# Kernel tuning notes

Measured on AMD Instinct MI355X. Metric: run time of the kernel, lower is better.

Reference implementation:

```python
import jax, jax.numpy as jnp
import numpy as np

N, E, D_IN, D, D_OUT, L = 50000, 800000, 128, 256, 64, 3
TAU0 = 0.5
LN_EPS = 1e-5


def setup_inputs() -> dict:
    key = jax.random.key(0)
    ks = jax.random.split(key, 16)
    u01 = jax.random.uniform(ks[2], (L, 2, N, 2), minval=1e-6, maxval=1.0 - 1e-6)
    gumbel = -jnp.log(-jnp.log(u01))  # standard Gumbel(0,1) noise, one draw per layer per action net
    s = lambda k, shape, fan: jax.random.normal(k, shape) * np.float32(1.0 / np.sqrt(fan))
    return {
        'x': jax.random.normal(ks[0], (N, D_IN), dtype=jnp.float32),
        'edge_index': jax.random.randint(ks[1], (2, E), 0, N),
        'gumbel_noise': gumbel,
        'W_enc': s(ks[3], (D_IN, D), D_IN), 'b_enc': jnp.zeros((D,), jnp.float32),
        'W_root': s(ks[4], (L, D, D), D), 'W_agg': s(ks[5], (L, D, D), D), 'b_env': jnp.zeros((L, D), jnp.float32),
        'Wa_in_r': s(ks[6], (D, 2), D), 'Wa_in_a': s(ks[7], (D, 2), D), 'b_in': jnp.zeros((2,), jnp.float32),
        'Wa_out_r': s(ks[8], (D, 2), D), 'Wa_out_a': s(ks[9], (D, 2), D), 'b_out': jnp.zeros((2,), jnp.float32),
        'Wt_r': s(ks[10], (D, 1), D), 'Wt_a': s(ks[11], (D, 1), D), 'b_t': jnp.zeros((1,), jnp.float32),
        'ln_g': jnp.ones((D,), jnp.float32), 'ln_b': jnp.zeros((D,), jnp.float32),
        'W_dec': s(ks[12], (D, D_OUT), D), 'b_dec': jnp.zeros((D_OUT,), jnp.float32),
    }


def reference(x, edge_index, gumbel_noise, W_enc, b_enc, W_root, W_agg, b_env,
              Wa_in_r, Wa_in_a, b_in, Wa_out_r, Wa_out_a, b_out,
              Wt_r, Wt_a, b_t, ln_g, ln_b, W_dec, b_dec):
    n = x.shape[0]
    u, v = edge_index[0], edge_index[1]  # message flows v -> u (aggregate at u)

    def conv(h, Wr, Wa, b, ew=None):
        # GraphConv-style: root transform + sum-aggregated (optionally edge-weighted) neighbor transform
        msg = h[v] if ew is None else ew[:, None] * h[v]  # [E, D]
        agg = jax.ops.segment_sum(msg, u, num_segments=n)  # [N, D]
        return h @ Wr + agg @ Wa + b

    def layernorm(h):
        m = jnp.mean(h, axis=-1, keepdims=True)
        var = jnp.mean((h - m) ** 2, axis=-1, keepdims=True)
        return (h - m) * jax.lax.rsqrt(var + LN_EPS) * ln_g + ln_b

    def gumbel_hard(logits, g, temp):
        # hard gumbel-softmax with straight-through estimator, per-node temperature
        y = jax.nn.softmax((logits + g) / temp, axis=-1)
        hard = jax.nn.one_hot(jnp.argmax(y, axis=-1), 2, dtype=y.dtype)
        return hard + y - jax.lax.stop_gradient(y)

    # env encoder + (dropout=identity) + relu
    h = jax.nn.relu(x @ W_enc + b_enc)

    for l in range(W_root.shape[0]):
        h = layernorm(h)
        in_logits = conv(h, Wa_in_r, Wa_in_a, b_in)    # [N, 2]
        out_logits = conv(h, Wa_out_r, Wa_out_a, b_out)  # [N, 2]
        t = conv(h, Wt_r, Wt_a, b_t)                   # [N, 1]
        temp = 1.0 / (jax.nn.softplus(t) + TAU0)       # TempSoftPlus: per-node inverse temperature
        in_prob = gumbel_hard(in_logits, gumbel_noise[l, 0], temp)
        out_prob = gumbel_hard(out_logits, gumbel_noise[l, 1], temp)
        ew = in_prob[:, 0][u] * out_prob[:, 0][v]      # [E] gated edge weights
        h = jax.nn.relu(conv(h, W_root[l], W_agg[l], b_env[l], ew))

    h = layernorm(h)
    return h @ W_dec + b_dec
```

## Files before the change

### kernel.cpp

```cpp
#include <hip/hip_runtime.h>
#include <cstdint>

#define NN 50000
#define EE 800000
#define DIN 128
#define DD 256
#define DOUT 64
#define NLAYERS 3
#define LN_EPS 1e-5f
#define NB_SCAN ((NN + 255) / 256)

typedef __attribute__((ext_vector_type(8))) _Float16 h8;
typedef __attribute__((ext_vector_type(4))) _Float16 h4;
typedef __attribute__((ext_vector_type(4))) float f4;

__device__ __forceinline__ float red16(float v) {
  v += __shfl_xor(v, 1, 64);
  v += __shfl_xor(v, 2, 64);
  v += __shfl_xor(v, 4, 64);
  v += __shfl_xor(v, 8, 64);
  return v;
}

__device__ __forceinline__ void splith(const float4& a, const float4& b, h8& p1, h8& p2) {
  float t[8] = {a.x, a.y, a.z, a.w, b.x, b.y, b.z, b.w};
#pragma unroll
  for (int i = 0; i < 8; ++i) {
    _Float16 x = (_Float16)t[i];
    p1[i] = x;
    p2[i] = (_Float16)(t[i] - (float)x);
  }
}

__global__ void k_zero_deg(int* __restrict__ deg) {
  int i = blockIdx.x * 256 + threadIdx.x;
  if (i < NN) deg[i] = 0;
}

__global__ void k_deg(const int* __restrict__ ei, int* __restrict__ deg) {
  int e = blockIdx.x * 256 + threadIdx.x;
  if (e < EE) atomicAdd(&deg[ei[e]], 1);
}

__global__ __launch_bounds__(256) void k_scan1(const int* __restrict__ deg,
                                               int* __restrict__ bsum) {
  __shared__ int sm[256];
  const int t = threadIdx.x;
  int i = blockIdx.x * 256 + t;
  sm[t] = (i < NN) ? deg[i] : 0;
  __syncthreads();
  for (int off = 128; off > 0; off >>= 1) {
    if (t < off) sm[t] += sm[t + off];
    __syncthreads();
  }
  if (t == 0) bsum[blockIdx.x] = sm[0];
}

__global__ __launch_bounds__(256) void k_scan2(const int* __restrict__ bsum,
                                               int* __restrict__ boff,
                                               int* __restrict__ rowptr) {
  __shared__ int sm[256];
  const int t = threadIdx.x;
  int v = (t < NB_SCAN) ? bsum[t] : 0;
  sm[t] = v;
  __syncthreads();
  for (int off = 1; off < 256; off <<= 1) {
    int x = (t >= off) ? sm[t - off] : 0;
    __syncthreads();
    sm[t] += x;
    __syncthreads();
  }
  if (t < NB_SCAN) boff[t] = sm[t] - v;
  if (t == 0) rowptr[NN] = sm[255];
}

__global__ __launch_bounds__(256) void k_scan3(const int* __restrict__ deg,
                                               const int* __restrict__ boff,
                                               int* __restrict__ rowptr,
                                               int* __restrict__ cursor) {
  __shared__ int sm[256];
  const int t = threadIdx.x;
  int i = blockIdx.x * 256 + t;
  int v = (i < NN) ? deg[i] : 0;
  sm[t] = v;
  __syncthreads();
  for (int off = 1; off < 256; off <<= 1) {
    int x = (t >= off) ? sm[t - off] : 0;
    __syncthreads();
    sm[t] += x;
    __syncthreads();
  }
  if (i < NN) {
    int r = boff[blockIdx.x] + sm[t] - v;
    rowptr[i] = r;
    cursor[i] = r;
  }
}

__global__ void k_fill(const int* __restrict__ ei, int* __restrict__ cursor,
                       int* __restrict__ csr_v) {
  int e = blockIdx.x * 256 + threadIdx.x;
  if (e >= EE) return;
  int u = ei[e], v = ei[EE + e];
  int slot = atomicAdd(&cursor[u], 1);
  csr_v[slot] = v;
}

__global__ void k_prep_conv(const float* __restrict__ Wr, const float* __restrict__ Wa,
                            _Float16* __restrict__ W1, _Float16* __restrict__ W2) {
  int idx = blockIdx.x * 256 + threadIdx.x;
  if (idx >= NLAYERS * DD * 2 * DD) return;
  int l = idx >> 17;
  int rem = idx & 131071;
  int n = rem >> 9, k = rem & 511;
  float w = (k < DD) ? Wr[((size_t)l * DD + k) * DD + n]
                     : Wa[((size_t)l * DD + (k - DD)) * DD + n];
  _Float16 x = (_Float16)w;
  W1[idx] = x;
  W2[idx] = (_Float16)(w - (float)x);
}

__global__ void k_prep_ed(const float* __restrict__ We, const float* __restrict__ Wd,
                          _Float16* __restrict__ E1, _Float16* __restrict__ E2,
                          _Float16* __restrict__ D1, _Float16* __restrict__ D2) {
  int idx = blockIdx.x * 256 + threadIdx.x;
  if (idx < DIN * DD) {
    int n = idx / DIN, k = idx - n * DIN;
    float w = We[(size_t)k * DD + n];
    _Float16 x = (_Float16)w;
    E1[idx] = x;
    E2[idx] = (_Float16)(w - (float)x);
  } else if (idx < DIN * DD + DD * DOUT) {
    int j = idx - DIN * DD;
    int n = j / DD, k = j - n * DD;
    float w = Wd[(size_t)k * DOUT + n];
    _Float16 x = (_Float16)w;
    D1[j] = x;
    D2[j] = (_Float16)(w - (float)x);
  }
}

__global__ __launch_bounds__(256) void k_gates_csr(
    const int* __restrict__ rowptr, const int* __restrict__ csr_v,
    const float* __restrict__ SR, const float* __restrict__ SA,
    const float* __restrict__ gn, const float* __restrict__ b_in,
    const float* __restrict__ b_out, unsigned char* __restrict__ gin,
    unsigned char* __restrict__ gout, int l) {
  int u = blockIdx.x * 256 + threadIdx.x;
  if (u >= NN) return;
  int beg = rowptr[u], end = rowptr[u + 1];
  float4 a = make_float4(0.f, 0.f, 0.f, 0.f);
  for (int j = beg; j < end; ++j) {
    int v = csr_v[j];
    float4 s = *(const float4*)(SA + (size_t)v * 4);
    a.x += s.x; a.y += s.y; a.z += s.z; a.w += s.w;
  }
  float4 r = *(const float4*)(SR + (size_t)u * 4);
  const float* gi = gn + ((size_t)(l * 2 + 0) * NN + u) * 2;
  const float* go = gn + ((size_t)(l * 2 + 1) * NN + u) * 2;
  float li0 = r.x + a.x + b_in[0] + gi[0];
  float li1 = r.y + a.y + b_in[1] + gi[1];
  gin[u] = (li0 >= li1) ? 1 : 0;
  float lo0 = r.z + a.z + b_out[0] + go[0];
  float lo1 = r.w + a.w + b_out[1] + go[1];
  gout[u] = (lo0 >= lo1) ? 1 : 0;
}

__global__ __launch_bounds__(256) void k_wagg_csr(
    const int* __restrict__ rowptr, const int* __restrict__ csr_v,
    const unsigned char* __restrict__ gin, const unsigned char* __restrict__ gout,
    const _Float16* __restrict__ hn1, const _Float16* __restrict__ hn2,
    _Float16* __restrict__ agg1, _Float16* __restrict__ agg2) {
  const int lane = threadIdx.x & 63;
  const int u = blockIdx.x * 4 + (threadIdx.x >> 6);
  if (u >= NN) return;
  float4 acc = make_float4(0.f, 0.f, 0.f, 0.f);
  float4 acc2 = make_float4(0.f, 0.f, 0.f, 0.f);
  if (gin[u]) {
    int beg = rowptr[u], end = rowptr[u + 1];
    for (int j0 = beg; j0 < end; j0 += 64) {
      int rem = end - j0;
      int v = -1;
      if (lane < rem) v = csr_v[j0 + lane];
      int ok = (v >= 0) ? (int)gout[v] : 0;
      unsigned long long mask = __ballot(ok);
      while (mask) {
        int l0 = __builtin_ctzll(mask);
        mask &= mask - 1;
        int vv0 = __shfl(v, l0);
        const h4* p0a = (const h4*)(hn1 + (size_t)vv0 * DD + lane * 4);
        const h4* p0b = (const h4*)(hn2 + (size_t)vv0 * DD + lane * 4);
        if (mask) {
          int l1 = __builtin_ctzll(mask);
          mask &= mask - 1;
          int vv1 = __shfl(v, l1);
          const h4* p1a = (const h4*)(hn1 + (size_t)vv1 * DD + lane * 4);
          const h4* p1b = (const h4*)(hn2 + (size_t)vv1 * DD + lane * 4);
          h4 a0 = *p0a, b0 = *p0b, a1 = *p1a, b1 = *p1b;
          acc.x += (float)a0[0] + (float)b0[0]; acc.y += (float)a0[1] + (float)b0[1];
          acc.z += (float)a0[2] + (float)b0[2]; acc.w += (float)a0[3] + (float)b0[3];
          acc2.x += (float)a1[0] + (float)b1[0]; acc2.y += (float)a1[1] + (float)b1[1];
          acc2.z += (float)a1[2] + (float)b1[2]; acc2.w += (float)a1[3] + (float)b1[3];
        } else {
          h4 a0 = *p0a, b0 = *p0b;
          acc.x += (float)a0[0] + (float)b0[0]; acc.y += (float)a0[1] + (float)b0[1];
          acc.z += (float)a0[2] + (float)b0[2]; acc.w += (float)a0[3] + (float)b0[3];
        }
      }
    }
    acc.x += acc2.x; acc.y += acc2.y; acc.z += acc2.z; acc.w += acc2.w;
  }
  {
    float t[4] = {acc.x, acc.y, acc.z, acc.w};
    h4 q1, q2;
#pragma unroll
    for (int i = 0; i < 4; ++i) {
      _Float16 x = (_Float16)t[i];
      q1[i] = x;
      q2[i] = (_Float16)(t[i] - (float)x);
    }
    *(h4*)(agg1 + (size_t)u * DD + lane * 4) = q1;
    *(h4*)(agg2 + (size_t)u * DD + lane * 4) = q2;
  }
}

#define LDPh 40

template <int KTOT, int NFN, bool FUSE_LN, bool AFP32, bool DUAL, bool RELU>
__global__ __launch_bounds__(256, 3) void k_gemm(
    const float* __restrict__ Af,
    const _Float16* __restrict__ A1a, const _Float16* __restrict__ A2a,
    const _Float16* __restrict__ A1b, const _Float16* __restrict__ A2b,
    const _Float16* __restrict__ B1, const _Float16* __restrict__ B2,
    const float* __restrict__ bias,
    const float* __restrict__ lng, const float* __restrict__ lnb,
    const float* __restrict__ Wir, const float* __restrict__ Wia,
    const float* __restrict__ Wor, const float* __restrict__ Woa,
    _Float16* __restrict__ O1, _Float16* __restrict__ O2,
    float* __restrict__ SR, float* __restrict__ SA,
    float* __restrict__ Of, int ostr) {
  constexpr int BN = NFN * 32;
  constexpr int KSTEPS = KTOT / 32;
  constexpr int NBR = BN / 64;
  constexpr int AS = AFP32 ? KTOT : DD;
  __shared__ _Float16 smem[(64 + BN) * LDPh * 2];
  _Float16* sA1 = smem;
  _Float16* sA2 = sA1 + 64 * LDPh;
  _Float16* sB1 = sA2 + 64 * LDPh;
  _Float16* sB2 = sB1 + BN * LDPh;

  const int tid = threadIdx.x;
  const int lane = tid & 63, w = tid >> 6;
  const int wr = w >> 1, wc = w & 1;
  const int fr = lane & 15, g4 = lane >> 4;
  const int fs = g4 * 8;
  const int i0 = blockIdx.x * 64;

  const int ar = tid >> 2, ak = (tid & 3) * 8;
  int garow = i0 + ar;
  if (garow >= NN) garow = NN - 1;
  const size_t aoff = (size_t)garow * AS;

  f4 acc[2][NFN];
#pragma unroll
  for (int mi = 0; mi < 2; ++mi)
#pragma unroll
    for (int ni = 0; ni < NFN; ++ni) acc[mi][ni] = (f4){0.f, 0.f, 0.f, 0.f};

  float4 fa0, fa1;
  h8 ra1, ra2;
  h8 rb1[NBR], rb2[NBR];
  {
    if constexpr (AFP32) {
      const float* pa = Af + aoff + ak;
      fa0 = *(const float4*)(pa);
      fa1 = *(const float4*)(pa + 4);
    } else {
      ra1 = *(const h8*)(A1a + aoff + ak);
      ra2 = *(const h8*)(A2a + aoff + ak);
    }
#pragma unroll
    for (int i = 0; i < NBR; ++i) {
      size_t bo = (size_t)(ar + i * 64) * KTOT + ak;
      rb1[i] = *(const h8*)(B1 + bo);
      rb2[i] = *(const h8*)(B2 + bo);
    }
  }
  for (int kt = 0; kt < KSTEPS; ++kt) {
    __syncthreads();
    {
      int o = ar * LDPh + ak;
      if constexpr (AFP32) {
        h8 p1, p2;
        splith(fa0, fa1, p1, p2);
        *(h8*)&sA1[o] = p1;
        *(h8*)&sA2[o] = p2;
      } else {
        *(h8*)&sA1[o] = ra1;
        *(h8*)&sA2[o] = ra2;
      }
#pragma unroll
      for (int i = 0; i < NBR; ++i) {
        int ob = (ar + i * 64) * LDPh + ak;
        *(h8*)&sB1[ob] = rb1[i];
        *(h8*)&sB2[ob] = rb2[i];
      }
    }
    __syncthreads();
    if (kt < KSTEPS - 1) {
      int kb = (kt + 1) * 32;
      if constexpr (AFP32) {
        const float* pa = Af + aoff + kb + ak;
        fa0 = *(const float4*)(pa);
        fa1 = *(const float4*)(pa + 4);
      } else {
        const _Float16 *p1, *p2;
        int ko;
        if constexpr (DUAL) {
          bool lo = kb < DD;
          p1 = lo ? A1a : A1b;
          p2 = lo ? A2a : A2b;
          ko = lo ? kb : kb - DD;
        } else {
          p1 = A1a; p2 = A2a; ko = kb;
        }
        ra1 = *(const h8*)(p1 + aoff + ko + ak);
        ra2 = *(const h8*)(p2 + aoff + ko + ak);
      }
#pragma unroll
      for (int i = 0; i < NBR; ++i) {
        size_t bo = (size_t)(ar + i * 64) * KTOT + kb + ak;
        rb1[i] = *(const h8*)(B1 + bo);
        rb2[i] = *(const h8*)(B2 + bo);
      }
    }
    h8 a1[2], a2[2];
#pragma unroll
    for (int mi = 0; mi < 2; ++mi) {
      int r = (wr * 32 + mi * 16 + fr) * LDPh + fs;
      a1[mi] = *(const h8*)&sA1[r];
      a2[mi] = *(const h8*)&sA2[r];
    }
#pragma unroll
    for (int ni = 0; ni < NFN; ++ni) {
      int c = (wc * (NFN * 16) + ni * 16 + fr) * LDPh + fs;
      h8 b1 = *(const h8*)&sB1[c];
      h8 b2 = *(const h8*)&sB2[c];
#pragma unroll
      for (int mi = 0; mi < 2; ++mi) {
        acc[mi][ni] = __builtin_amdgcn_mfma_f32_16x16x32_f16(a1[mi], b1, acc[mi][ni], 0, 0, 0);
        acc[mi][ni] = __builtin_amdgcn_mfma_f32_16x16x32_f16(a1[mi], b2, acc[mi][ni], 0, 0, 0);
        acc[mi][ni] = __builtin_amdgcn_mfma_f32_16x16x32_f16(a2[mi], b1, acc[mi][ni], 0, 0, 0);
      }
    }
  }

  if constexpr (FUSE_LN) {
    __syncthreads();
    float* rsum = (float*)smem;
    float* rsq = rsum + 128;
    float* rdots = rsq + 128;
#pragma unroll
    for (int mi = 0; mi < 2; ++mi)
#pragma unroll
      for (int ni = 0; ni < NFN; ++ni) {
        int col = wc * 128 + ni * 16 + fr;
        float bv = bias[col];
#pragma unroll
        for (int r = 0; r < 4; ++r) {
          float v = acc[mi][ni][r] + bv;
          if constexpr (RELU) v = fmaxf(v, 0.f);
          acc[mi][ni][r] = v;
        }
      }
#pragma unroll
    for (int mi = 0; mi < 2; ++mi)
#pragma unroll
      for (int r = 0; r < 4; ++r) {
        float s = 0.f, q = 0.f;
#pragma unroll
        for (int ni = 0; ni < NFN; ++ni) {
          float v = acc[mi][ni][r];
          s += v;
          q += v * v;
        }
        s = red16(s);
        q = red16(q);
        if (fr == 0) {
          int rl = wr * 32 + mi * 16 + g4 * 4 + r;
          rsum[rl * 2 + wc] = s;
          rsq[rl * 2 + wc] = q;
        }
      }
    __syncthreads();
    float mv[2][4], rv[2][4];
#pragma unroll
    for (int mi = 0; mi < 2; ++mi)
#pragma unroll
      for (int r = 0; r < 4; ++r) {
        int rl = wr * 32 + mi * 16 + g4 * 4 + r;
        float S = rsum[rl * 2] + rsum[rl * 2 + 1];
        float Q = rsq[rl * 2] + rsq[rl * 2 + 1];
        float m = S * (1.f / DD);
        float var = fmaxf(Q * (1.f / DD) - m * m, 0.f);
        mv[mi][r] = m;
        rv[mi][r] = 1.f / sqrtf(var + LN_EPS);
      }
#pragma unroll
    for (int mi = 0; mi < 2; ++mi)
#pragma unroll
      for (int ni = 0; ni < NFN; ++ni) {
        int col = wc * 128 + ni * 16 + fr;
        float g = lng[col], b = lnb[col];
#pragma unroll
        for (int r = 0; r < 4; ++r) {
          float o = (acc[mi][ni][r] - mv[mi][r]) * rv[mi][r] * g + b;
          acc[mi][ni][r] = o;
          int row = i0 + wr * 32 + mi * 16 + g4 * 4 + r;
          if (row < NN) {
            _Float16 x = (_Float16)o;
            O1[(size_t)row * DD + col] = x;
            O2[(size_t)row * DD + col] = (_Float16)(o - (float)x);
          }
        }
      }
#pragma unroll
    for (int mi = 0; mi < 2; ++mi) {
      float pd[4][8];
#pragma unroll
      for (int r = 0; r < 4; ++r)
#pragma unroll
        for (int j = 0; j < 8; ++j) pd[r][j] = 0.f;
#pragma unroll
      for (int ni = 0; ni < NFN; ++ni) {
        int col = wc * 128 + ni * 16 + fr;
        float2 wir = *(const float2*)(Wir + col * 2);
        float2 wia = *(const float2*)(Wia + col * 2);
        float2 wor = *(const float2*)(Wor + col * 2);
        float2 woa = *(const float2*)(Woa + col * 2);
#pragma unroll
        for (int r = 0; r < 4; ++r) {
          float o = acc[mi][ni][r];
          pd[r][0] = fmaf(o, wir.x, pd[r][0]);
          pd[r][1] = fmaf(o, wir.y, pd[r][1]);
          pd[r][2] = fmaf(o, wia.x, pd[r][2]);
          pd[r][3] = fmaf(o, wia.y, pd[r][3]);
          pd[r][4] = fmaf(o, wor.x, pd[r][4]);
          pd[r][5] = fmaf(o, wor.y, pd[r][5]);
          pd[r][6] = fmaf(o, woa.x, pd[r][6]);
          pd[r][7] = fmaf(o, woa.y, pd[r][7]);
        }
      }
#pragma unroll
      for (int r = 0; r < 4; ++r)
#pragma unroll
        for (int j = 0; j < 8; ++j) pd[r][j] = red16(pd[r][j]);
      if (fr == 0) {
#pragma unroll
        for (int r = 0; r < 4; ++r) {
          int rl = wr * 32 + mi * 16 + g4 * 4 + r;
#pragma unroll
          for (int j = 0; j < 8; ++j) rdots[(rl * 2 + wc) * 8 + j] = pd[r][j];
        }
      }
    }
    __syncthreads();
    if (tid < 64) {
      int row = i0 + tid;
      if (row < NN) {
        float d[8];
#pragma unroll
        for (int j = 0; j < 8; ++j) d[j] = rdots[tid * 16 + j] + rdots[tid * 16 + 8 + j];
        *(float4*)(SR + (size_t)row * 4) = make_float4(d[0], d[1], d[4], d[5]);
        *(float4*)(SA + (size_t)row * 4) = make_float4(d[2], d[3], d[6], d[7]);
      }
    }
  } else {
#pragma unroll
    for (int mi = 0; mi < 2; ++mi)
#pragma unroll
      for (int ni = 0; ni < NFN; ++ni) {
        int col = wc * (NFN * 16) + ni * 16 + fr;
        float bv = bias[col];
#pragma unroll
        for (int r = 0; r < 4; ++r) {
          int row = i0 + wr * 32 + mi * 16 + g4 * 4 + r;
          if (row < NN) Of[(size_t)row * ostr + col] = acc[mi][ni][r] + bv;
        }
      }
  }
}

extern "C" void kernel_launch(void* const* d_in, const int* in_sizes, int n_in,
                              void* d_out, int out_size, void* d_ws, size_t ws_size,
                              hipStream_t stream) {
  const float* x = (const float*)d_in[0];
  const int* ei = (const int*)d_in[1];
  const float* gn = (const float*)d_in[2];
  const float* W_enc = (const float*)d_in[3];
  const float* b_enc = (const float*)d_in[4];
  const float* W_root = (const float*)d_in[5];
  const float* W_agg = (const float*)d_in[6];
  const float* b_env = (const float*)d_in[7];
  const float* Wa_in_r = (const float*)d_in[8];
  const float* Wa_in_a = (const float*)d_in[9];
  const float* b_in = (const float*)d_in[10];
  const float* Wa_out_r = (const float*)d_in[11];
  const float* Wa_out_a = (const float*)d_in[12];
  const float* b_out = (const float*)d_in[13];
  const float* ln_g = (const float*)d_in[17];
  const float* ln_b = (const float*)d_in[18];
  const float* W_dec = (const float*)d_in[19];
  const float* b_dec = (const float*)d_in[20];
  float* out = (float*)d_out;

  float* ws = (float*)d_ws;
  size_t off = 0;
  _Float16* hnA1 = (_Float16*)(ws + off); off += (size_t)NN * DD / 2;
  _Float16* hnA2 = (_Float16*)(ws + off); off += (size_t)NN * DD / 2;
  _Float16* hnB1 = (_Float16*)(ws + off); off += (size_t)NN * DD / 2;
  _Float16* hnB2 = (_Float16*)(ws + off); off += (size_t)NN * DD / 2;
  _Float16* agg1 = (_Float16*)(ws + off); off += (size_t)NN * DD / 2;
  _Float16* agg2 = (_Float16*)(ws + off); off += (size_t)NN * DD / 2;
  float* SR = ws + off; off += (size_t)NN * 4;
  float* SA = ws + off; off += (size_t)NN * 4;
  int* rowptr = (int*)(ws + off); off += (size_t)NN + 4;
  int* csr_v = (int*)(ws + off);  off += (size_t)EE;
  unsigned char* gin = (unsigned char*)(ws + off);  off += (size_t)NN / 4;
  unsigned char* gout = (unsigned char*)(ws + off); off += (size_t)NN / 4;
  _Float16* cW1 = (_Float16*)(ws + off); off += (size_t)NLAYERS * DD * DD;
  _Float16* cW2 = (_Float16*)(ws + off); off += (size_t)NLAYERS * DD * DD;
  _Float16* eW1 = (_Float16*)(ws + off); off += (size_t)DD * DIN / 2;
  _Float16* eW2 = (_Float16*)(ws + off); off += (size_t)DD * DIN / 2;
  _Float16* dW1 = (_Float16*)(ws + off); off += (size_t)DOUT * DD / 2;
  _Float16* dW2 = (_Float16*)(ws + off); off += (size_t)DOUT * DD / 2;
  if (ws_size < off * sizeof(float)) return;
  int* deg = (int*)SR;
  int* bsum = (int*)SR + NN;
  int* boffp = (int*)SR + NN + 256;
  int* cursor = (int*)SA;

  k_zero_deg<<<(NN + 255) / 256, 256, 0, stream>>>(deg);
  k_deg<<<(EE + 255) / 256, 256, 0, stream>>>(ei, deg);
  k_scan1<<<NB_SCAN, 256, 0, stream>>>(deg, bsum);
  k_scan2<<<1, 256, 0, stream>>>(bsum, boffp, rowptr);
  k_scan3<<<NB_SCAN, 256, 0, stream>>>(deg, boffp, rowptr, cursor);
  k_fill<<<(EE + 255) / 256, 256, 0, stream>>>(ei, cursor, csr_v);

  k_prep_conv<<<(NLAYERS * DD * 2 * DD + 255) / 256, 256, 0, stream>>>(W_root, W_agg, cW1, cW2);
  k_prep_ed<<<(DIN * DD + DD * DOUT + 255) / 256, 256, 0, stream>>>(W_enc, W_dec,
                                                                    eW1, eW2, dW1, dW2);

  const int gb = (NN + 63) / 64;
  k_gemm<DIN, 8, true, true, false, true><<<gb, 256, 0, stream>>>(
      x, nullptr, nullptr, nullptr, nullptr, eW1, eW2, b_enc,
      ln_g, ln_b, Wa_in_r, Wa_in_a, Wa_out_r, Wa_out_a,
      hnA1, hnA2, SR, SA, nullptr, 0);

  _Float16 *cur1 = hnA1, *cur2 = hnA2, *nxt1 = hnB1, *nxt2 = hnB2;
  for (int l = 0; l < NLAYERS; ++l) {
    k_gates_csr<<<(NN + 255) / 256, 256, 0, stream>>>(rowptr, csr_v, SR, SA, gn,
                                                      b_in, b_out, gin, gout, l);
    k_wagg_csr<<<(NN + 3) / 4, 256, 0, stream>>>(rowptr, csr_v, gin, gout,
                                                 cur1, cur2, agg1, agg2);
    k_gemm<2 * DD, 8, true, false, true, true><<<gb, 256, 0, stream>>>(
        nullptr, cur1, cur2, agg1, agg2,
        cW1 + (size_t)l * DD * 2 * DD, cW2 + (size_t)l * DD * 2 * DD,
        b_env + (size_t)l * DD,
        ln_g, ln_b, Wa_in_r, Wa_in_a, Wa_out_r, Wa_out_a,
        nxt1, nxt2, SR, SA, nullptr, 0);
    _Float16* t1 = cur1; cur1 = nxt1; nxt1 = t1;
    _Float16* t2 = cur2; cur2 = nxt2; nxt2 = t2;
  }

  k_gemm<DD, 2, false, false, false, false><<<gb, 256, 0, stream>>>(
      nullptr, cur1, cur2, nullptr, nullptr, dW1, dW2, b_dec,
      nullptr, nullptr, nullptr, nullptr, nullptr, nullptr,
      nullptr, nullptr, nullptr, nullptr, out, DOUT);
}
```

Baseline: 781.8 us.

## Enlarge fused GEMM tile to 128 rows with 512-thread blocks, split decoder kernel

The fused GEMM+LayerNorm kernel now uses 128-row tiles with 8 waves (2x4 layout), each wave computing a 64x64 sub-tile with a 4x4 MFMA accumulator array. Each loaded B tile is therefore reused across twice as many rows, and LDS reads of A/B fragments are amortised over more MFMAs. The decoder GEMM moves into its own specialised kernel. The trade-off is higher register pressure (64 accumulators per lane plus the epilogue arrays) under launch_bounds(512,4), and fewer blocks (391) across the CUs.

```diff
diff --git a/kernel.cpp b/kernel.cpp
--- a/kernel.cpp
+++ b/kernel.cpp
@@ -226,8 +226,8 @@
 
 #define LDPh 40
 
-template <int KTOT, int NFN, bool FUSE_LN, bool AFP32, bool DUAL, bool RELU>
-__global__ __launch_bounds__(256, 3) void k_gemm(
+template <int KTOT, bool AFP32, bool DUAL, bool RELU>
+__global__ __launch_bounds__(512, 4) void k_gemm_fused(
     const float* __restrict__ Af,
     const _Float16* __restrict__ A1a, const _Float16* __restrict__ A2a,
     const _Float16* __restrict__ A1b, const _Float16* __restrict__ A2b,
@@ -237,39 +237,38 @@
     const float* __restrict__ Wir, const float* __restrict__ Wia,
     const float* __restrict__ Wor, const float* __restrict__ Woa,
     _Float16* __restrict__ O1, _Float16* __restrict__ O2,
-    float* __restrict__ SR, float* __restrict__ SA,
-    float* __restrict__ Of, int ostr) {
-  constexpr int BN = NFN * 32;
+    float* __restrict__ SR, float* __restrict__ SA) {
   constexpr int KSTEPS = KTOT / 32;
-  constexpr int NBR = BN / 64;
   constexpr int AS = AFP32 ? KTOT : DD;
-  __shared__ _Float16 smem[(64 + BN) * LDPh * 2];
+  __shared__ _Float16 smem[(128 + 256) * LDPh * 2];
   _Float16* sA1 = smem;
-  _Float16* sA2 = sA1 + 64 * LDPh;
-  _Float16* sB1 = sA2 + 64 * LDPh;
-  _Float16* sB2 = sB1 + BN * LDPh;
+  _Float16* sA2 = sA1 + 128 * LDPh;
+  _Float16* sB1 = sA2 + 128 * LDPh;
+  _Float16* sB2 = sB1 + 256 * LDPh;
 
   const int tid = threadIdx.x;
-  const int lane = tid & 63, w = tid >> 6;
-  const int wr = w >> 1, wc = w & 1;
+  const int lane = tid & 63, wid = tid >> 6;
+  const int wr = wid >> 2, wcq = wid & 3;
   const int fr = lane & 15, g4 = lane >> 4;
   const int fs = g4 * 8;
-  const int i0 = blockIdx.x * 64;
+  const int i0 = blockIdx.x * 128;
 
   const int ar = tid >> 2, ak = (tid & 3) * 8;
   int garow = i0 + ar;
   if (garow >= NN) garow = NN - 1;
   const size_t aoff = (size_t)garow * AS;
-
-  f4 acc[2][NFN];
-#pragma unroll
-  for (int mi = 0; mi < 2; ++mi)
-#pragma unroll
-    for (int ni = 0; ni < NFN; ++ni) acc[mi][ni] = (f4){0.f, 0.f, 0.f, 0.f};
+  const int br = tid >> 1, bk = (tid & 1) * 16;
+  const size_t boff = (size_t)br * KTOT + bk;
+
+  f4 acc[4][4];
+#pragma unroll
+  for (int mi = 0; mi < 4; ++mi)
+#pragma unroll
+    for (int ni = 0; ni < 4; ++ni) acc[mi][ni] = (f4){0.f, 0.f, 0.f, 0.f};
 
   float4 fa0, fa1;
   h8 ra1, ra2;
-  h8 rb1[NBR], rb2[NBR];
+  h8 rb1a, rb1b, rb2a, rb2b;
   {
     if constexpr (AFP32) {
       const float* pa = Af + aoff + ak;
@@ -279,32 +278,29 @@
       ra1 = *(const h8*)(A1a + aoff + ak);
       ra2 = *(const h8*)(A2a + aoff + ak);
     }
-#pragma unroll
-    for (int i = 0; i < NBR; ++i) {
-      size_t bo = (size_t)(ar + i * 64) * KTOT + ak;
-      rb1[i] = *(const h8*)(B1 + bo);
-      rb2[i] = *(const h8*)(B2 + bo);
-    }
+    rb1a = *(const h8*)(B1 + boff);
+    rb1b = *(const h8*)(B1 + boff + 8);
+    rb2a = *(const h8*)(B2 + boff);
+    rb2b = *(const h8*)(B2 + boff + 8);
   }
   for (int kt = 0; kt < KSTEPS; ++kt) {
     __syncthreads();
     {
-      int o = ar * LDPh + ak;
+      int oa = ar * LDPh + ak;
       if constexpr (AFP32) {
         h8 p1, p2;
         splith(fa0, fa1, p1, p2);
-        *(h8*)&sA1[o] = p1;
-        *(h8*)&sA2[o] = p2;
+        *(h8*)&sA1[oa] = p1;
+        *(h8*)&sA2[oa] = p2;
       } else {
-        *(h8*)&sA1[o] = ra1;
-        *(h8*)&sA2[o] = ra2;
-      }
-#pragma unroll
-      for (int i = 0; i < NBR; ++i) {
-        int ob = (ar + i * 64) * LDPh + ak;
-        *(h8*)&sB1[ob] = rb1[i];
-        *(h8*)&sB2[ob] = rb2[i];
-      }
+        *(h8*)&sA1[oa] = ra1;
+        *(h8*)&sA2[oa] = ra2;
+      }
+      int ob = br * LDPh + bk;
+      *(h8*)&sB1[ob] = rb1a;
+      *(h8*)&sB1[ob + 8] = rb1b;
+      *(h8*)&sB2[ob] = rb2a;
+      *(h8*)&sB2[ob + 8] = rb2b;
     }
     __syncthreads();
     if (kt < KSTEPS - 1) {
@@ -327,168 +323,240 @@
         ra1 = *(const h8*)(p1 + aoff + ko + ak);
         ra2 = *(const h8*)(p2 + aoff + ko + ak);
       }
-#pragma unroll
-      for (int i = 0; i < NBR; ++i) {
-        size_t bo = (size_t)(ar + i * 64) * KTOT + kb + ak;
-        rb1[i] = *(const h8*)(B1 + bo);
-        rb2[i] = *(const h8*)(B2 + bo);
-      }
-    }
-    h8 a1[2], a2[2];
-#pragma unroll
-    for (int mi = 0; mi < 2; ++mi) {
-      int r = (wr * 32 + mi * 16 + fr) * LDPh + fs;
-      a1[mi] = *(const h8*)&sA1[r];
-      a2[mi] = *(const h8*)&sA2[r];
-    }
-#pragma unroll
-    for (int ni = 0; ni < NFN; ++ni) {
-      int c = (wc * (NFN * 16) + ni * 16 + fr) * LDPh + fs;
+      rb1a = *(const h8*)(B1 + boff + kb);
+      rb1b = *(const h8*)(B1 + boff + kb + 8);
+      rb2a = *(const h8*)(B2 + boff + kb);
+      rb2b = *(const h8*)(B2 + boff + kb + 8);
+    }
+    h8 b1[4], b2[4];
+#pragma unroll
+    for (int ni = 0; ni < 4; ++ni) {
+      int c = (wcq * 64 + ni * 16 + fr) * LDPh + fs;
+      b1[ni] = *(const h8*)&sB1[c];
+      b2[ni] = *(const h8*)&sB2[c];
+    }
+#pragma unroll
+    for (int mi = 0; mi < 4; ++mi) {
+      int r = (wr * 64 + mi * 16 + fr) * LDPh + fs;
+      {
+        h8 a1 = *(const h8*)&sA1[r];
+#pragma unroll
+        for (int ni = 0; ni < 4; ++ni) {
+          acc[mi][ni] = __builtin_amdgcn_mfma_f32_16x16x32_f16(a1, b1[ni], acc[mi][ni], 0, 0, 0);
+          acc[mi][ni] = __builtin_amdgcn_mfma_f32_16x16x32_f16(a1, b2[ni], acc[mi][ni], 0, 0, 0);
+        }
+      }
+      {
+        h8 a2 = *(const h8*)&sA2[r];
+#pragma unroll
+        for (int ni = 0; ni < 4; ++ni)
+          acc[mi][ni] = __builtin_amdgcn_mfma_f32_16x16x32_f16(a2, b1[ni], acc[mi][ni], 0, 0, 0);
+      }
+    }
+  }
+
+  __syncthreads();
+  float* rsum = (float*)smem;
+  float* rsq = rsum + 512;
+  float* rdots = rsq + 512;
+#pragma unroll
+  for (int mi = 0; mi < 4; ++mi)
+#pragma unroll
+    for (int ni = 0; ni < 4; ++ni) {
+      int col = wcq * 64 + ni * 16 + fr;
+      float bv = bias[col];
+#pragma unroll
+      for (int r = 0; r < 4; ++r) {
+        float v = acc[mi][ni][r] + bv;
+        if constexpr (RELU) v = fmaxf(v, 0.f);
+        acc[mi][ni][r] = v;
+      }
+    }
+#pragma unroll
+  for (int mi = 0; mi < 4; ++mi)
+#pragma unroll
+    for (int r = 0; r < 4; ++r) {
+      float s = 0.f, q = 0.f;
+#pragma unroll
+      for (int ni = 0; ni < 4; ++ni) {
+        float v = acc[mi][ni][r];
+        s += v;
+        q += v * v;
+      }
+      s = red16(s);
+      q = red16(q);
+      if (fr == 0) {
+        int rl = wr * 64 + mi * 16 + g4 * 4 + r;
+        rsum[rl * 4 + wcq] = s;
+        rsq[rl * 4 + wcq] = q;
+      }
+    }
+  __syncthreads();
+  float mv[4][4], rv[4][4];
+#pragma unroll
+  for (int mi = 0; mi < 4; ++mi)
+#pragma unroll
+    for (int r = 0; r < 4; ++r) {
+      int rl = wr * 64 + mi * 16 + g4 * 4 + r;
+      float S = rsum[rl * 4] + rsum[rl * 4 + 1] + rsum[rl * 4 + 2] + rsum[rl * 4 + 3];
+      float Q = rsq[rl * 4] + rsq[rl * 4 + 1] + rsq[rl * 4 + 2] + rsq[rl * 4 + 3];
+      float m = S * (1.f / DD);
+      float var = fmaxf(Q * (1.f / DD) - m * m, 0.f);
+      mv[mi][r] = m;
+      rv[mi][r] = 1.f / sqrtf(var + LN_EPS);
+    }
+#pragma unroll
+  for (int mi = 0; mi < 4; ++mi)
+#pragma unroll
+    for (int ni = 0; ni < 4; ++ni) {
+      int col = wcq * 64 + ni * 16 + fr;
+      float g = lng[col], b = lnb[col];
+#pragma unroll
+      for (int r = 0; r < 4; ++r) {
+        float o = (acc[mi][ni][r] - mv[mi][r]) * rv[mi][r] * g + b;
+        acc[mi][ni][r] = o;
+        int row = i0 + wr * 64 + mi * 16 + g4 * 4 + r;
+        if (row < NN) {
+          _Float16 x = (_Float16)o;
+          O1[(size_t)row * DD + col] = x;
+          O2[(size_t)row * DD + col] = (_Float16)(o - (float)x);
+        }
+      }
+    }
+#pragma unroll
+  for (int mi = 0; mi < 4; ++mi) {
+    float pd[4][8];
+#pragma unroll
+    for (int r = 0; r < 4; ++r)
+#pragma unroll
+      for (int j = 0; j < 8; ++j) pd[r][j] = 0.f;
+#pragma unroll
+    for (int ni = 0; ni < 4; ++ni) {
+      int col = wcq * 64 + ni * 16 + fr;
+      float2 wir = *(const float2*)(Wir + col * 2);
+      float2 wia = *(const float2*)(Wia + col * 2);
+      float2 wor = *(const float2*)(Wor + col * 2);
+      float2 woa = *(const float2*)(Woa + col * 2);
+#pragma unroll
+      for (int r = 0; r < 4; ++r) {
+        float o = acc[mi][ni][r];
+        pd[r][0] = fmaf(o, wir.x, pd[r][0]);
+        pd[r][1] = fmaf(o, wir.y, pd[r][1]);
+        pd[r][2] = fmaf(o, wia.x, pd[r][2]);
+        pd[r][3] = fmaf(o, wia.y, pd[r][3]);
+        pd[r][4] = fmaf(o, wor.x, pd[r][4]);
+        pd[r][5] = fmaf(o, wor.y, pd[r][5]);
+        pd[r][6] = fmaf(o, woa.x, pd[r][6]);
+        pd[r][7] = fmaf(o, woa.y, pd[r][7]);
+      }
+    }
+#pragma unroll
+    for (int r = 0; r < 4; ++r)
+#pragma unroll
+      for (int j = 0; j < 8; ++j) pd[r][j] = red16(pd[r][j]);
+    if (fr == 0) {
+#pragma unroll
+      for (int r = 0; r < 4; ++r) {
+        int rl = wr * 64 + mi * 16 + g4 * 4 + r;
+#pragma unroll
+        for (int j = 0; j < 8; ++j) rdots[(rl * 4 + wcq) * 8 + j] = pd[r][j];
+      }
+    }
+  }
+  __syncthreads();
+  if (tid < 128) {
+    int row = i0 + tid;
+    if (row < NN) {
+      float d[8];
+#pragma unroll
+      for (int j = 0; j < 8; ++j)
+        d[j] = rdots[(tid * 4 + 0) * 8 + j] + rdots[(tid * 4 + 1) * 8 + j] +
+               rdots[(tid * 4 + 2) * 8 + j] + rdots[(tid * 4 + 3) * 8 + j];
+      *(float4*)(SR + (size_t)row * 4) = make_float4(d[0], d[1], d[4], d[5]);
+      *(float4*)(SA + (size_t)row * 4) = make_float4(d[2], d[3], d[6], d[7]);
+    }
+  }
+}
+
+__global__ __launch_bounds__(256, 3) void k_decoder(
+    const _Float16* __restrict__ A1, const _Float16* __restrict__ A2,
+    const _Float16* __restrict__ B1, const _Float16* __restrict__ B2,
+    const float* __restrict__ bias, float* __restrict__ Of) {
+  constexpr int KTOT = DD;
+  constexpr int KSTEPS = KTOT / 32;
+  __shared__ _Float16 smem[(64 + 64) * LDPh * 2];
+  _Float16* sA1 = smem;
+  _Float16* sA2 = sA1 + 64 * LDPh;
+  _Float16* sB1 = sA2 + 64 * LDPh;
+  _Float16* sB2 = sB1 + 64 * LDPh;
+  const int tid = threadIdx.x;
+  const int lane = tid & 63, w = tid >> 6;
+  const int wr = w >> 1, wc = w & 1;
+  const int fr = lane & 15, g4 = lane >> 4;
+  const int fs = g4 * 8;
+  const int i0 = blockIdx.x * 64;
+  const int ar = tid >> 2, ak = (tid & 3) * 8;
+  int garow = i0 + ar;
+  if (garow >= NN) garow = NN - 1;
+  const size_t aoff = (size_t)garow * DD;
+  const size_t boff = (size_t)ar * KTOT + ak;
+
+  f4 acc[2][2];
+#pragma unroll
+  for (int mi = 0; mi < 2; ++mi)
+#pragma unroll
+    for (int ni = 0; ni < 2; ++ni) acc[mi][ni] = (f4){0.f, 0.f, 0.f, 0.f};
+
+  h8 ra1, ra2, rb1, rb2;
+  ra1 = *(const h8*)(A1 + aoff + ak);
+  ra2 = *(const h8*)(A2 + aoff + ak);
+  rb1 = *(const h8*)(B1 + boff);
+  rb2 = *(const h8*)(B2 + boff);
+  for (int kt = 0; kt < KSTEPS; ++kt) {
+    __syncthreads();
+    {
+      int o = ar * LDPh + ak;
+      *(h8*)&sA1[o] = ra1;
+      *(h8*)&sA2[o] = ra2;
+      *(h8*)&sB1[o] = rb1;
+      *(h8*)&sB2[o] = rb2;
+    }
+    __syncthreads();
+    if (kt < KSTEPS - 1) {
+      int kb = (kt + 1) * 32;
+      ra1 = *(const h8*)(A1 + aoff + kb + ak);
+      ra2 = *(const h8*)(A2 + aoff + kb + ak);
+      rb1 = *(const h8*)(B1 + boff + kb);
+      rb2 = *(const h8*)(B2 + boff + kb);
+    }
+#pragma unroll
+    for (int ni = 0; ni < 2; ++ni) {
+      int c = (wc * 32 + ni * 16 + fr) * LDPh + fs;
       h8 b1 = *(const h8*)&sB1[c];
       h8 b2 = *(const h8*)&sB2[c];
 #pragma unroll
       for (int mi = 0; mi < 2; ++mi) {
-        acc[mi][ni] = __builtin_amdgcn_mfma_f32_16x16x32_f16(a1[mi], b1, acc[mi][ni], 0, 0, 0);
-        acc[mi][ni] = __builtin_amdgcn_mfma_f32_16x16x32_f16(a1[mi], b2, acc[mi][ni], 0, 0, 0);
-        acc[mi][ni] = __builtin_amdgcn_mfma_f32_16x16x32_f16(a2[mi], b1, acc[mi][ni], 0, 0, 0);
-      }
-    }
-  }
-
-  if constexpr (FUSE_LN) {
-    __syncthreads();
-    float* rsum = (float*)smem;
-    float* rsq = rsum + 128;
-    float* rdots = rsq + 128;
-#pragma unroll
-    for (int mi = 0; mi < 2; ++mi)
-#pragma unroll
-      for (int ni = 0; ni < NFN; ++ni) {
-        int col = wc * 128 + ni * 16 + fr;
-        float bv = bias[col];
-#pragma unroll
-        for (int r = 0; r < 4; ++r) {
-          float v = acc[mi][ni][r] + bv;
-          if constexpr (RELU) v = fmaxf(v, 0.f);
-          acc[mi][ni][r] = v;
-        }
-      }
-#pragma unroll
-    for (int mi = 0; mi < 2; ++mi)
+        int r = (wr * 32 + mi * 16 + fr) * LDPh + fs;
+        h8 a1 = *(const h8*)&sA1[r];
+        h8 a2 = *(const h8*)&sA2[r];
+        acc[mi][ni] = __builtin_amdgcn_mfma_f32_16x16x32_f16(a1, b1, acc[mi][ni], 0, 0, 0);
+        acc[mi][ni] = __builtin_amdgcn_mfma_f32_16x16x32_f16(a1, b2, acc[mi][ni], 0, 0, 0);
+        acc[mi][ni] = __builtin_amdgcn_mfma_f32_16x16x32_f16(a2, b1, acc[mi][ni], 0, 0, 0);
+      }
+    }
+  }
+#pragma unroll
+  for (int mi = 0; mi < 2; ++mi)
+#pragma unroll
+    for (int ni = 0; ni < 2; ++ni) {
+      int col = wc * 32 + ni * 16 + fr;
+      float bv = bias[col];
 #pragma unroll
       for (int r = 0; r < 4; ++r) {
-        float s = 0.f, q = 0.f;
-#pragma unroll
-        for (int ni = 0; ni < NFN; ++ni) {
-          float v = acc[mi][ni][r];
-          s += v;
-          q += v * v;
-        }
-        s = red16(s);
-        q = red16(q);
-        if (fr == 0) {
-          int rl = wr * 32 + mi * 16 + g4 * 4 + r;
-          rsum[rl * 2 + wc] = s;
-          rsq[rl * 2 + wc] = q;
-        }
-      }
-    __syncthreads();
-    float mv[2][4], rv[2][4];
-#pragma unroll
-    for (int mi = 0; mi < 2; ++mi)
-#pragma unroll
-      for (int r = 0; r < 4; ++r) {
-        int rl = wr * 32 + mi * 16 + g4 * 4 + r;
-        float S = rsum[rl * 2] + rsum[rl * 2 + 1];
-        float Q = rsq[rl * 2] + rsq[rl * 2 + 1];
-        float m = S * (1.f / DD);
-        float var = fmaxf(Q * (1.f / DD) - m * m, 0.f);
-        mv[mi][r] = m;
-        rv[mi][r] = 1.f / sqrtf(var + LN_EPS);
-      }
-#pragma unroll
-    for (int mi = 0; mi < 2; ++mi)
-#pragma unroll
-      for (int ni = 0; ni < NFN; ++ni) {
-        int col = wc * 128 + ni * 16 + fr;
-        float g = lng[col], b = lnb[col];
-#pragma unroll
-        for (int r = 0; r < 4; ++r) {
-          float o = (acc[mi][ni][r] - mv[mi][r]) * rv[mi][r] * g + b;
-          acc[mi][ni][r] = o;
-          int row = i0 + wr * 32 + mi * 16 + g4 * 4 + r;
-          if (row < NN) {
-            _Float16 x = (_Float16)o;
-            O1[(size_t)row * DD + col] = x;
-            O2[(size_t)row * DD + col] = (_Float16)(o - (float)x);
-          }
-        }
-      }
-#pragma unroll
-    for (int mi = 0; mi < 2; ++mi) {
-      float pd[4][8];
-#pragma unroll
-      for (int r = 0; r < 4; ++r)
-#pragma unroll
-        for (int j = 0; j < 8; ++j) pd[r][j] = 0.f;
-#pragma unroll
-      for (int ni = 0; ni < NFN; ++ni) {
-        int col = wc * 128 + ni * 16 + fr;
-        float2 wir = *(const float2*)(Wir + col * 2);
-        float2 wia = *(const float2*)(Wia + col * 2);
-        float2 wor = *(const float2*)(Wor + col * 2);
-        float2 woa = *(const float2*)(Woa + col * 2);
-#pragma unroll
-        for (int r = 0; r < 4; ++r) {
-          float o = acc[mi][ni][r];
-          pd[r][0] = fmaf(o, wir.x, pd[r][0]);
-          pd[r][1] = fmaf(o, wir.y, pd[r][1]);
-          pd[r][2] = fmaf(o, wia.x, pd[r][2]);
-          pd[r][3] = fmaf(o, wia.y, pd[r][3]);
-          pd[r][4] = fmaf(o, wor.x, pd[r][4]);
-          pd[r][5] = fmaf(o, wor.y, pd[r][5]);
-          pd[r][6] = fmaf(o, woa.x, pd[r][6]);
-          pd[r][7] = fmaf(o, woa.y, pd[r][7]);
-        }
-      }
-#pragma unroll
-      for (int r = 0; r < 4; ++r)
-#pragma unroll
-        for (int j = 0; j < 8; ++j) pd[r][j] = red16(pd[r][j]);
-      if (fr == 0) {
-#pragma unroll
-        for (int r = 0; r < 4; ++r) {
-          int rl = wr * 32 + mi * 16 + g4 * 4 + r;
-#pragma unroll
-          for (int j = 0; j < 8; ++j) rdots[(rl * 2 + wc) * 8 + j] = pd[r][j];
-        }
-      }
-    }
-    __syncthreads();
-    if (tid < 64) {
-      int row = i0 + tid;
-      if (row < NN) {
-        float d[8];
-#pragma unroll
-        for (int j = 0; j < 8; ++j) d[j] = rdots[tid * 16 + j] + rdots[tid * 16 + 8 + j];
-        *(float4*)(SR + (size_t)row * 4) = make_float4(d[0], d[1], d[4], d[5]);
-        *(float4*)(SA + (size_t)row * 4) = make_float4(d[2], d[3], d[6], d[7]);
-      }
-    }
-  } else {
-#pragma unroll
-    for (int mi = 0; mi < 2; ++mi)
-#pragma unroll
-      for (int ni = 0; ni < NFN; ++ni) {
-        int col = wc * (NFN * 16) + ni * 16 + fr;
-        float bv = bias[col];
-#pragma unroll
-        for (int r = 0; r < 4; ++r) {
-          int row = i0 + wr * 32 + mi * 16 + g4 * 4 + r;
-          if (row < NN) Of[(size_t)row * ostr + col] = acc[mi][ni][r] + bv;
-        }
-      }
-  }
+        int row = i0 + wr * 32 + mi * 16 + g4 * 4 + r;
+        if (row < NN) Of[(size_t)row * DOUT + col] = acc[mi][ni][r] + bv;
+      }
+    }
 }
 
 extern "C" void kernel_launch(void* const* d_in, const int* in_sizes, int n_in,
@@ -551,11 +619,11 @@
   k_prep_ed<<<(DIN * DD + DD * DOUT + 255) / 256, 256, 0, stream>>>(W_enc, W_dec,
                                                                     eW1, eW2, dW1, dW2);
 
-  const int gb = (NN + 63) / 64;
-  k_gemm<DIN, 8, true, true, false, true><<<gb, 256, 0, stream>>>(
+  const int gb128 = (NN + 127) / 128;
+  k_gemm_fused<DIN, true, false, true><<<gb128, 512, 0, stream>>>(
       x, nullptr, nullptr, nullptr, nullptr, eW1, eW2, b_enc,
       ln_g, ln_b, Wa_in_r, Wa_in_a, Wa_out_r, Wa_out_a,
-      hnA1, hnA2, SR, SA, nullptr, 0);
+      hnA1, hnA2, SR, SA);
 
   _Float16 *cur1 = hnA1, *cur2 = hnA2, *nxt1 = hnB1, *nxt2 = hnB2;
   for (int l = 0; l < NLAYERS; ++l) {
@@ -563,18 +631,15 @@
                                                       b_in, b_out, gin, gout, l);
     k_wagg_csr<<<(NN + 3) / 4, 256, 0, stream>>>(rowptr, csr_v, gin, gout,
                                                  cur1, cur2, agg1, agg2);
-    k_gemm<2 * DD, 8, true, false, true, true><<<gb, 256, 0, stream>>>(
+    k_gemm_fused<2 * DD, false, true, true><<<gb128, 512, 0, stream>>>(
         nullptr, cur1, cur2, agg1, agg2,
         cW1 + (size_t)l * DD * 2 * DD, cW2 + (size_t)l * DD * 2 * DD,
         b_env + (size_t)l * DD,
         ln_g, ln_b, Wa_in_r, Wa_in_a, Wa_out_r, Wa_out_a,
-        nxt1, nxt2, SR, SA, nullptr, 0);
+        nxt1, nxt2, SR, SA);
     _Float16* t1 = cur1; cur1 = nxt1; nxt1 = t1;
     _Float16* t2 = cur2; cur2 = nxt2; nxt2 = t2;
   }
 
-  k_gemm<DD, 2, false, false, false, false><<<gb, 256, 0, stream>>>(
-      nullptr, cur1, cur2, nullptr, nullptr, dW1, dW2, b_dec,
-      nullptr, nullptr, nullptr, nullptr, nullptr, nullptr,
-      nullptr, nullptr, nullptr, nullptr, out, DOUT);
-}
+  k_decoder<<<(NN + 63) / 64, 256, 0, stream>>>(cur1, cur2, dW1, dW2, b_dec, out);
+}
```

Result: slower. 942.1 us (+20.5%).
